# Kernel tuning notes

Measured on AMD Instinct MI355X. Metric: run time of the kernel, lower is better.

The kernel has to match this reference:

```python
import jax, jax.numpy as jnp
import numpy as np

N = 120_000      # points
D = 64           # voxel grid resolution per axis
HID = 96         # hidden_dim
IN = 96          # input_dim
C = HID + IN     # 192, conv input channels
EPS = 1e-5       # BatchNorm eps


def _build_geometry(rng):
    """Precompute the hash-map lookups torchsparse builds on the fly."""
    pts = rng.uniform(0, D - 1e-3, size=(N, 3)).astype(np.float32)
    vox = np.floor(pts).astype(np.int64)                      # voxel coord per point
    flat = (vox[:, 0] * D + vox[:, 1]) * D + vox[:, 2]
    uniq, seg = np.unique(flat, return_inverse=True)          # occupied voxels
    M = uniq.shape[0]
    lut = -np.ones(D * D * D, dtype=np.int64)
    lut[uniq] = np.arange(M)
    ux, uy, uz = uniq // (D * D), (uniq // D) % D, uniq % D
    # 27 kernel offsets for the 3x3x3 sparse conv
    offs = np.array([(dx, dy, dz) for dx in (-1, 0, 1)
                     for dy in (-1, 0, 1) for dz in (-1, 0, 1)], dtype=np.int64)
    nx = ux[:, None] + offs[None, :, 0]
    ny = uy[:, None] + offs[None, :, 1]
    nz = uz[:, None] + offs[None, :, 2]
    ok = (nx >= 0) & (nx < D) & (ny >= 0) & (ny < D) & (nz >= 0) & (nz < D)
    nflat = (np.clip(nx, 0, D - 1) * D + np.clip(ny, 0, D - 1)) * D + np.clip(nz, 0, D - 1)
    nbr = np.where(ok, lut[nflat], -1)
    nbr = np.where(nbr < 0, M, nbr).astype(np.int32)          # row M = zero pad
    # 8 trilinear corners for devoxelization
    frac = pts - vox
    coffs = np.array([(a, b, c) for a in (0, 1) for b in (0, 1) for c in (0, 1)], dtype=np.int64)
    cx = vox[:, 0:1] + coffs[None, :, 0]
    cy = vox[:, 1:2] + coffs[None, :, 1]
    cz = vox[:, 2:3] + coffs[None, :, 2]
    okc = (cx < D) & (cy < D) & (cz < D)
    cflat = (np.clip(cx, 0, D - 1) * D + np.clip(cy, 0, D - 1)) * D + np.clip(cz, 0, D - 1)
    cidx = np.where(okc, lut[cflat], -1)
    w = np.ones((N, 8), dtype=np.float32)
    for k in range(8):
        for d in range(3):
            w[:, k] *= frac[:, d] if coffs[k, d] == 1 else (1.0 - frac[:, d])
    w = np.where(cidx >= 0, w, 0.0).astype(np.float32)        # missing voxel -> weight 0
    cidx = np.where(cidx < 0, M, cidx).astype(np.int32)
    return seg.astype(np.int32), nbr, cidx, w


def setup_inputs() -> dict:
    rng = np.random.default_rng(0)
    seg, nbr, cidx, cw = _build_geometry(rng)
    key = jax.random.key(0)
    ks = jax.random.split(key, 4)
    return {
        "hidden_F": jax.random.normal(ks[0], (N, HID), jnp.float32),
        "query_F": jax.random.normal(ks[1], (N, IN), jnp.float32),
        "W_conv": jax.random.normal(ks[2], (27, C, HID), jnp.float32) * (1.0 / np.sqrt(27.0 * C)),
        "gamma": jnp.ones((HID,), jnp.float32),
        "beta": jnp.zeros((HID,), jnp.float32),
        "W_lin": jax.random.normal(ks[3], (C, IN), jnp.float32) * (1.0 / np.sqrt(C)),
        "b_lin": jnp.zeros((IN,), jnp.float32),
        "corner_w": jnp.asarray(cw),
        "seg_ids": jnp.asarray(seg),
        "nbr_idx": jnp.asarray(nbr),
        "corner_idx": jnp.asarray(cidx),
    }


def reference(hidden_F, query_F, W_conv, gamma, beta, W_lin, b_lin, corner_w,
              seg_ids, nbr_idx, corner_idx):
    M = nbr_idx.shape[0]
    hx = jnp.concatenate([hidden_F, query_F], axis=1)                  # [N, C]
    # initial_voxelize: scatter-mean point features into occupied voxels
    vsum = jax.ops.segment_sum(hx, seg_ids, num_segments=M)            # [M, C]
    cnt = jax.ops.segment_sum(jnp.ones((hx.shape[0], 1), hx.dtype),
                              seg_ids, num_segments=M)
    vfeat = vsum / jnp.maximum(cnt, 1.0)
    # sparse 3x3x3 conv: gather 27 hashed neighbors (row M is zero pad)
    vpad = jnp.concatenate([vfeat, jnp.zeros((1, C), vfeat.dtype)], axis=0)
    acc = jnp.zeros((M, HID), vfeat.dtype)
    for k in range(27):  # fixed small kernel loop
        acc = acc + vpad[nbr_idx[:, k]] @ W_conv[k]
    # BatchNorm (batch stats over occupied voxels) + ReLU
    mu = jnp.mean(acc, axis=0)
    var = jnp.mean((acc - mu) ** 2, axis=0)
    y = jax.nn.relu(gamma * (acc - mu) * jax.lax.rsqrt(var + EPS) + beta)
    # voxel_to_point(nearest=False): trilinear 8-corner gather
    ypad = jnp.concatenate([y, jnp.zeros((1, HID), y.dtype)], axis=0)
    out = jnp.zeros((hx.shape[0], HID), y.dtype)
    for k in range(8):  # fixed corner loop
        out = out + corner_w[:, k:k + 1] * ypad[corner_idx[:, k]]
    # residual point transform: out.F + Linear(hx.F)
    return out + hx @ W_lin + b_lin
```

## Files before the change

### kernel.cpp

```cpp
#include <hip/hip_runtime.h>
#include <hip/hip_bf16.h>
#include <cstdint>

typedef __bf16 bf16;
typedef __bf16 bf16x8 __attribute__((ext_vector_type(8)));
typedef __bf16 bf16x4 __attribute__((ext_vector_type(4)));
typedef float f32x4 __attribute__((ext_vector_type(4)));
typedef int i32x4 __attribute__((ext_vector_type(4)));

#define HIDC 96
#define CINC 192
#define EPSC 1e-5f

#define STG_B 20480
#define STG_ELEM 10240

#define GLD_LDS16(g, l)                                                        \
  __builtin_amdgcn_global_load_lds(                                            \
      (const __attribute__((address_space(1))) void*)(g),                      \
      (__attribute__((address_space(3))) void*)(l), 16, 0, 0)

__global__ void k_repack(const float* __restrict__ Wc, const float* __restrict__ Wl,
                         bf16* __restrict__ dst, int total) {
  int t = blockIdx.x * 256 + threadIdx.x;
  if (t >= total) return;
  int off = t / 18432;
  int rem = t - off * 18432;
  int cix = rem >> 9;
  int lane = (rem >> 3) & 63;
  int j = rem & 7;
  int k = (cix / 6) * 32 + ((lane >> 4) << 3) + j;
  int col = (cix % 6) * 16 + (lane & 15);
  const float* src = (off < 27) ? (Wc + ((size_t)off * CINC + k) * HIDC + col)
                                : (Wl + (size_t)k * HIDC + col);
  int half = (cix >= 18) ? 1 : 0;
  size_t de = (size_t)(off * 2 + half) * STG_ELEM + (size_t)(rem - half * 9216);
  dst[de] = (bf16)(*src);
}

__global__ void k_count(const int* __restrict__ seg, int* __restrict__ cnt, int Npts) {
  int t = blockIdx.x * 256 + threadIdx.x;
  if (t < Npts) atomicAdd(cnt + seg[t], 1);
}

__global__ void k_bsum(const int* __restrict__ cnt, int* __restrict__ bsum, int M) {
  __shared__ int sm[256];
  int i = blockIdx.x * 256 + threadIdx.x;
  sm[threadIdx.x] = (i < M) ? cnt[i] : 0;
  __syncthreads();
  for (int st = 128; st > 0; st >>= 1) {
    if (threadIdx.x < st) sm[threadIdx.x] += sm[threadIdx.x + st];
    __syncthreads();
  }
  if (threadIdx.x == 0) bsum[blockIdx.x] = sm[0];
}

__global__ void k_bscan(int* __restrict__ bsum, int nb) {
  __shared__ int sm[1024];
  int i = threadIdx.x;
  int v = (i < nb) ? bsum[i] : 0;
  sm[i] = v;
  __syncthreads();
  for (int st = 1; st < 1024; st <<= 1) {
    int t = (i >= st) ? sm[i - st] : 0;
    __syncthreads();
    sm[i] += t;
    __syncthreads();
  }
  if (i < nb) bsum[i] = sm[i] - v;
}

__global__ void k_ptr(const int* __restrict__ cnt, const int* __restrict__ bsum,
                      int* __restrict__ ptr, int* __restrict__ cursor, int M) {
  __shared__ int sm[256];
  int i = blockIdx.x * 256 + threadIdx.x;
  int v = (i < M) ? cnt[i] : 0;
  sm[threadIdx.x] = v;
  __syncthreads();
  for (int st = 1; st < 256; st <<= 1) {
    int t = (threadIdx.x >= st) ? sm[threadIdx.x - st] : 0;
    __syncthreads();
    sm[threadIdx.x] += t;
    __syncthreads();
  }
  if (i < M) {
    int e = bsum[blockIdx.x] + sm[threadIdx.x] - v;
    ptr[i] = e;
    cursor[i] = e;
  }
}

__global__ void k_scatter(const int* __restrict__ seg, int* __restrict__ cursor,
                          int* __restrict__ plist, int Npts) {
  int t = blockIdx.x * 256 + threadIdx.x;
  if (t < Npts) {
    int pos = atomicAdd(cursor + seg[t], 1);
    plist[pos] = t;
  }
}

__global__ void k_gmean(const float* __restrict__ hid, const float* __restrict__ qry,
                        const int* __restrict__ ptr, const int* __restrict__ cnt,
                        const int* __restrict__ plist, bf16* __restrict__ vpad, int M) {
  int t = blockIdx.x * 256 + threadIdx.x;
  if (t >= (M + 1) * 48) return;
  int v = t / 48;
  int q = t - v * 48;
  f32x4 a = {0.f, 0.f, 0.f, 0.f};
  if (v < M) {
    int st = ptr[v], n = cnt[v];
    const float* base = (q < 24) ? (hid + q * 4) : (qry + (q - 24) * 4);
    for (int j = 0; j < n; j++) {
      int p = plist[st + j];
      a += *(const f32x4*)(base + (size_t)p * HIDC);
    }
    a *= (1.0f / (float)(n > 0 ? n : 1));
  }
  bf16x4 o;
#pragma unroll
  for (int j = 0; j < 4; j++) o[j] = (bf16)a[j];
  *(bf16x4*)(vpad + (size_t)v * CINC + q * 4) = o;
}

__launch_bounds__(256, 4)
__global__ void k_conv(const bf16* __restrict__ vpad, const int* __restrict__ nbr,
                       const bf16* __restrict__ wpack, float* __restrict__ accbuf,
                       float* __restrict__ bnsum, int M, int nblk, int nper) {
  const int bx = (int)(blockIdx.x & 7) * nper + (int)(blockIdx.x >> 3);
  if (bx >= nblk) return;
  __shared__ __align__(16) char smem[40960];
  const int tid = threadIdx.x;
  const int wave = tid >> 6;
  const int lane = tid & 63;
  const int m = lane & 15;
  const int quad = lane >> 4;
  const int rb = bx * 128 + wave * 32;

  f32x4 acc[2][6];
#pragma unroll
  for (int rt = 0; rt < 2; rt++)
#pragma unroll
    for (int ct = 0; ct < 6; ct++) {
      f32x4 z = {0.f, 0.f, 0.f, 0.f};
      acc[rt][ct] = z;
    }

  const char* wb = (const char*)wpack;

  {
    char* dstb = smem;
#pragma unroll
    for (int i = 0; i < 5; i++) {
      const int base = wave * 1024 + i * 4096;
      GLD_LDS16(wb + base + lane * 16, dstb + base);
    }
  }
  int gidx[2], gidx2[2];
#pragma unroll
  for (int rt = 0; rt < 2; rt++) {
    int r = rb + rt * 16 + m;
    gidx[rt] = (r < M) ? nbr[(size_t)r * 27] : M;
  }
  bf16x8 afn[2][3];
#pragma unroll
  for (int kc2 = 0; kc2 < 3; kc2++)
#pragma unroll
    for (int rt = 0; rt < 2; rt++)
      afn[rt][kc2] = *(const bf16x8*)(vpad + (size_t)gidx[rt] * CINC + kc2 * 32 + quad * 8);
  __builtin_amdgcn_s_barrier();

  for (int s = 0; s < 54; s++) {
    const int buf = s & 1;
    const int half = s & 1;
    const int off = s >> 1;
    if (half == 0) {
      const int offn = off + 1;
#pragma unroll
      for (int rt = 0; rt < 2; rt++) {
        int r = rb + rt * 16 + m;
        gidx2[rt] = (r < M && offn < 27) ? nbr[(size_t)r * 27 + offn] : M;
      }
    }
    if (s < 53) {
      const char* src = wb + (size_t)(s + 1) * STG_B;
      char* dstb = smem + (buf ^ 1) * STG_B;
#pragma unroll
      for (int i = 0; i < 5; i++) {
        const int base = wave * 1024 + i * 4096;
        GLD_LDS16(src + base + lane * 16, dstb + base);
      }
    }
    __builtin_amdgcn_sched_barrier(0);

    bf16x8 afc[2][3];
#pragma unroll
    for (int kc2 = 0; kc2 < 3; kc2++)
#pragma unroll
      for (int rt = 0; rt < 2; rt++) afc[rt][kc2] = afn[rt][kc2];

    const char* bbr = smem + buf * STG_B;
#pragma unroll
    for (int kc2 = 0; kc2 < 3; kc2++) {
#pragma unroll
      for (int ct = 0; ct < 6; ct++) {
        bf16x8 bfm = *(const bf16x8*)(bbr + (size_t)(kc2 * 6 + ct) * 1024 + (size_t)lane * 16);
#pragma unroll
        for (int rt = 0; rt < 2; rt++)
          acc[rt][ct] = __builtin_amdgcn_mfma_f32_16x16x32_bf16(afc[rt][kc2], bfm, acc[rt][ct], 0, 0, 0);
      }
      if (s < 53) {
        if (half == 0) {
#pragma unroll
          for (int rt = 0; rt < 2; rt++)
            afn[rt][kc2] = *(const bf16x8*)(vpad + (size_t)gidx[rt] * CINC +
                                            (kc2 + 3) * 32 + quad * 8);
        } else {
#pragma unroll
          for (int rt = 0; rt < 2; rt++)
            afn[rt][kc2] = *(const bf16x8*)(vpad + (size_t)gidx2[rt] * CINC +
                                            kc2 * 32 + quad * 8);
        }
      }
    }
    if (half == 1) {
      gidx[0] = gidx2[0];
      gidx[1] = gidx2[1];
    }
    asm volatile("s_waitcnt vmcnt(6)" ::: "memory");
    __builtin_amdgcn_s_barrier();
  }

  float ps[6], pq[6];
#pragma unroll
  for (int ct = 0; ct < 6; ct++) { ps[ct] = 0.f; pq[ct] = 0.f; }
#pragma unroll
  for (int rt = 0; rt < 2; rt++)
#pragma unroll
    for (int rr = 0; rr < 4; rr++) {
      const int r2 = rb + rt * 16 + quad * 4 + rr;
      if (r2 < M) {
#pragma unroll
        for (int ct = 0; ct < 6; ct++) {
          float v = acc[rt][ct][rr];
          ps[ct] += v;
          pq[ct] += v * v;
        }
      }
    }
#pragma unroll
  for (int ct = 0; ct < 6; ct++) {
    float s1 = ps[ct], s2 = pq[ct];
    s1 += __shfl_xor(s1, 16);
    s2 += __shfl_xor(s2, 16);
    s1 += __shfl_xor(s1, 32);
    s2 += __shfl_xor(s2, 32);
    if (quad == 0) {
      atomicAdd(bnsum + ct * 16 + m, s1);
      atomicAdd(bnsum + 96 + ct * 16 + m, s2);
    }
  }
  float(*trw)[98] = (float(*)[98])(smem + wave * (16 * 98 * 4));
  const int erow = lane >> 3;
  const int ecb = (lane & 7) * 4;
#pragma unroll
  for (int rt = 0; rt < 2; rt++) {
#pragma unroll
    for (int ct = 0; ct < 6; ct++)
#pragma unroll
      for (int rr = 0; rr < 4; rr++)
        trw[quad * 4 + rr][ct * 16 + m] = acc[rt][ct][rr];
#pragma unroll
    for (int rh = 0; rh < 2; rh++) {
      const int row = rh * 8 + erow;
      const int r2 = rb + rt * 16 + row;
      if (r2 < M) {
#pragma unroll
        for (int it = 0; it < 3; it++) {
          f32x4 v = *(const f32x4*)&trw[row][it * 32 + ecb];
          *(f32x4*)(accbuf + (size_t)r2 * HIDC + it * 32 + ecb) = v;
        }
      }
    }
  }
}

__global__ void k_bnapply(const float* __restrict__ accbuf, const float* __restrict__ bnsum,
                          const float* __restrict__ gamma, const float* __restrict__ beta,
                          bf16* __restrict__ ypad, int M) {
  __shared__ float ssc[96], ssh[96];
  if (threadIdx.x < 96) {
    int c = threadIdx.x;
    float inv = 1.0f / (float)M;
    float mu = bnsum[c] * inv;
    float var = fmaxf(bnsum[96 + c] * inv - mu * mu, 0.f);
    float sc = gamma[c] * rsqrtf(var + EPSC);
    ssc[c] = sc;
    ssh[c] = beta[c] - mu * sc;
  }
  __syncthreads();
  int t = blockIdx.x * 256 + threadIdx.x;
  if (t >= (M + 1) * 24) return;
  int v = t / 24;
  int g = t - v * 24;
  f32x4 y = {0.f, 0.f, 0.f, 0.f};
  if (v < M) {
    f32x4 a = *(const f32x4*)(accbuf + (size_t)v * HIDC + g * 4);
#pragma unroll
    for (int j = 0; j < 4; j++) y[j] = fmaxf(a[j] * ssc[g * 4 + j] + ssh[g * 4 + j], 0.f);
  }
  bf16x4 o;
#pragma unroll
  for (int j = 0; j < 4; j++) o[j] = (bf16)y[j];
  *(bf16x4*)(ypad + (size_t)v * HIDC + g * 4) = o;
}

__launch_bounds__(256, 4)
__global__ void k_linear(const float* __restrict__ hid, const float* __restrict__ qry,
                         const bf16* __restrict__ wlpack, const float* __restrict__ blin,
                         bf16* __restrict__ lin, int Npts) {
  const int tid = threadIdx.x;
  const int wave = tid >> 6;
  const int lane = tid & 63;
  const int m = lane & 15;
  const int quad = lane >> 4;
  const int rb = blockIdx.x * 128 + wave * 32;

  f32x4 acc[2][6];
#pragma unroll
  for (int rt = 0; rt < 2; rt++)
#pragma unroll
    for (int ct = 0; ct < 6; ct++) {
      f32x4 z = {0.f, 0.f, 0.f, 0.f};
      acc[rt][ct] = z;
    }

  int prow[2];
#pragma unroll
  for (int rt = 0; rt < 2; rt++) {
    int r = rb + rt * 16 + m;
    prow[rt] = (r < Npts) ? r : (Npts - 1);
  }
  const char* wp = (const char*)wlpack;
#pragma unroll
  for (int kc = 0; kc < 6; kc++) {
    const float* srcA = (kc < 3) ? (hid + kc * 32) : (qry + (kc - 3) * 32);
    bf16x8 af[2];
#pragma unroll
    for (int rt = 0; rt < 2; rt++) {
      const float* pA = srcA + (size_t)prow[rt] * HIDC + quad * 8;
      f32x4 lo = *(const f32x4*)pA;
      f32x4 hi = *(const f32x4*)(pA + 4);
#pragma unroll
      for (int j = 0; j < 4; j++) {
        af[rt][j] = (bf16)lo[j];
        af[rt][4 + j] = (bf16)hi[j];
      }
    }
    const int half = (kc >= 3) ? 1 : 0;
    const int kcl = kc - half * 3;
#pragma unroll
    for (int ct = 0; ct < 6; ct++) {
      bf16x8 bfm = *(const bf16x8*)(wp + (size_t)half * STG_B +
                                    (size_t)((kcl * 6 + ct) * 64 + lane) * 16);
#pragma unroll
      for (int rt = 0; rt < 2; rt++)
        acc[rt][ct] = __builtin_amdgcn_mfma_f32_16x16x32_bf16(af[rt], bfm, acc[rt][ct], 0, 0, 0);
    }
  }
  float bl[6];
#pragma unroll
  for (int ct = 0; ct < 6; ct++) bl[ct] = blin[ct * 16 + m];
#pragma unroll
  for (int rt = 0; rt < 2; rt++)
#pragma unroll
    for (int rr = 0; rr < 4; rr++) {
      const int r2 = rb + rt * 16 + quad * 4 + rr;
      if (r2 < Npts) {
        bf16* dst = lin + (size_t)r2 * HIDC + m;
#pragma unroll
        for (int ct = 0; ct < 6; ct++)
          dst[ct * 16] = (bf16)(acc[rt][ct][rr] + bl[ct]);
      }
    }
}

__global__ void k_out(const bf16* __restrict__ lin, const bf16* __restrict__ ypad,
                      const float* __restrict__ cw, const int* __restrict__ cidx,
                      float* __restrict__ out, int Npts) {
  int t = blockIdx.x * 256 + threadIdx.x;
  if (t >= Npts * 12) return;
  int p = t / 12;
  int g = t - p * 12;
  float a[8];
  bf16x8 lv = *(const bf16x8*)(lin + (size_t)p * HIDC + g * 8);
#pragma unroll
  for (int j = 0; j < 8; j++) a[j] = (float)lv[j];
  f32x4 w0 = *(const f32x4*)(cw + (size_t)p * 8);
  f32x4 w1 = *(const f32x4*)(cw + (size_t)p * 8 + 4);
  const i32x4* cp = (const i32x4*)(cidx + (size_t)p * 8);
  i32x4 c0 = cp[0], c1 = cp[1];
#pragma unroll
  for (int k = 0; k < 8; k++) {
    int idx = (k < 4) ? c0[k] : c1[k - 4];
    float wk = (k < 4) ? w0[k] : w1[k - 4];
    bf16x8 yv = *(const bf16x8*)(ypad + (size_t)idx * HIDC + g * 8);
#pragma unroll
    for (int j = 0; j < 8; j++) a[j] += wk * (float)yv[j];
  }
  float* op = out + (size_t)p * HIDC + g * 8;
  f32x4 s0, s1;
#pragma unroll
  for (int j = 0; j < 4; j++) { s0[j] = a[j]; s1[j] = a[4 + j]; }
  *(f32x4*)op = s0;
  *(f32x4*)(op + 4) = s1;
}

extern "C" void kernel_launch(void* const* d_in, const int* in_sizes, int n_in,
                              void* d_out, int out_size, void* d_ws, size_t ws_size,
                              hipStream_t stream) {
  const float* hid = (const float*)d_in[0];
  const float* qry = (const float*)d_in[1];
  const float* Wc = (const float*)d_in[2];
  const float* gamma = (const float*)d_in[3];
  const float* beta = (const float*)d_in[4];
  const float* Wl = (const float*)d_in[5];
  const float* blin = (const float*)d_in[6];
  const float* cw = (const float*)d_in[7];
  const int* seg = (const int*)d_in[8];
  const int* nbr = (const int*)d_in[9];
  const int* cidx = (const int*)d_in[10];
  float* out = (float*)d_out;
  const int Npts = in_sizes[0] / HIDC;
  const int M = in_sizes[9] / 27;

  char* ws = (char*)d_ws;
  size_t cur = 0;
  auto alloc = [&](size_t b) { size_t o = cur; cur = (cur + b + 255) & ~(size_t)255; return o; };
  size_t o_cnt = alloc((size_t)M * 4);
  size_t o_bn = alloc(192 * 4);
  size_t zend = cur;
  size_t o_ptr = alloc((size_t)M * 4);
  size_t o_cur = alloc((size_t)M * 4);
  size_t o_pl = alloc((size_t)Npts * 4);
  size_t o_bs = alloc(1024 * 4);
  size_t RA = (size_t)M * HIDC * 4;
  size_t needA = (size_t)Npts * HIDC * 2;
  if (needA > RA) RA = needA;
  size_t o_A = alloc(RA);
  size_t o_B = alloc((size_t)(M + 1) * CINC * 2);
  size_t o_wpack = alloc((size_t)56 * STG_B);
  (void)ws_size; (void)n_in; (void)out_size;

  int* cnt = (int*)(ws + o_cnt);
  float* bnsum = (float*)(ws + o_bn);
  int* ptr = (int*)(ws + o_ptr);
  int* cursor = (int*)(ws + o_cur);
  int* plist = (int*)(ws + o_pl);
  int* bsum = (int*)(ws + o_bs);
  float* accbuf = (float*)(ws + o_A);
  bf16* lin = (bf16*)(ws + o_A);
  bf16* vpad = (bf16*)(ws + o_B);
  bf16* ypad = (bf16*)(ws + o_B);
  bf16* wpack = (bf16*)(ws + o_wpack);
  bf16* wlpack = (bf16*)(ws + o_wpack + (size_t)54 * STG_B);

  hipMemsetAsync(ws, 0, zend, stream);

  int totalRepack = 28 * 18432;
  k_repack<<<(totalRepack + 255) / 256, 256, 0, stream>>>(Wc, Wl, wpack, totalRepack);

  int nb = (M + 255) / 256;
  k_count<<<(Npts + 255) / 256, 256, 0, stream>>>(seg, cnt, Npts);
  k_bsum<<<nb, 256, 0, stream>>>(cnt, bsum, M);
  k_bscan<<<1, 1024, 0, stream>>>(bsum, nb);
  k_ptr<<<nb, 256, 0, stream>>>(cnt, bsum, ptr, cursor, M);
  k_scatter<<<(Npts + 255) / 256, 256, 0, stream>>>(seg, cursor, plist, Npts);
  k_gmean<<<(((M + 1) * 48) + 255) / 256, 256, 0, stream>>>(hid, qry, ptr, cnt, plist, vpad, M);

  int nblk = (M + 127) / 128;
  int nper = (nblk + 7) / 8;
  k_conv<<<nper * 8, 256, 0, stream>>>(vpad, nbr, wpack, accbuf, bnsum, M, nblk, nper);
  k_bnapply<<<((M + 1) * 24 + 255) / 256, 256, 0, stream>>>(accbuf, bnsum, gamma, beta, ypad, M);
  k_linear<<<(Npts + 127) / 128, 256, 0, stream>>>(hid, qry, wlpack, blin, lin, Npts);
  k_out<<<(Npts * 12 + 255) / 256, 256, 0, stream>>>(lin, ypad, cw, cidx, out, Npts);
}
```

Before: 420.7 us.

## Stage conv weights through registers, scan with wave shuffles, store accumulators directly

The conv kernel stops using direct global-to-LDS loads for the weight stages. It now prefetches each stage into registers, writes it to a double-buffered LDS array, and syncs with __syncthreads. The accumulator write-out skips the LDS transpose and stores scalars straight to global memory, which gives less coalesced stores but no staging step. The block-sum scan is rewritten with wave shuffles instead of a shared-memory Hillis-Steele loop, and launch bounds drop to 3 waves per SIMD to allow more registers for the prefetch buffer.

```diff
diff --git a/kernel.cpp b/kernel.cpp
--- a/kernel.cpp
+++ b/kernel.cpp
@@ -14,11 +14,6 @@
 
 #define STG_B 20480
 #define STG_ELEM 10240
-
-#define GLD_LDS16(g, l)                                                        \
-  __builtin_amdgcn_global_load_lds(                                            \
-      (const __attribute__((address_space(1))) void*)(g),                      \
-      (__attribute__((address_space(3))) void*)(l), 16, 0, 0)
 
 __global__ void k_repack(const float* __restrict__ Wc, const float* __restrict__ Wl,
                          bf16* __restrict__ dst, int total) {
@@ -56,18 +51,29 @@
 }
 
 __global__ void k_bscan(int* __restrict__ bsum, int nb) {
-  __shared__ int sm[1024];
   int i = threadIdx.x;
   int v = (i < nb) ? bsum[i] : 0;
-  sm[i] = v;
+  int x = v;
+#pragma unroll
+  for (int d = 1; d < 64; d <<= 1) {
+    int t = __shfl_up(x, d);
+    if ((i & 63) >= d) x += t;
+  }
+  __shared__ int wsum[16];
+  if ((i & 63) == 63) wsum[i >> 6] = x;
   __syncthreads();
-  for (int st = 1; st < 1024; st <<= 1) {
-    int t = (i >= st) ? sm[i - st] : 0;
-    __syncthreads();
-    sm[i] += t;
-    __syncthreads();
-  }
-  if (i < nb) bsum[i] = sm[i] - v;
+  if (i < 16) {
+    int w = wsum[i];
+    int y = w;
+#pragma unroll
+    for (int d = 1; d < 16; d <<= 1) {
+      int t = __shfl_up(y, d, 16);
+      if (i >= d) y += t;
+    }
+    wsum[i] = y - w;
+  }
+  __syncthreads();
+  if (i < nb) bsum[i] = (x - v) + wsum[i >> 6];
 }
 
 __global__ void k_ptr(const int* __restrict__ cnt, const int* __restrict__ bsum,
@@ -122,13 +128,13 @@
   *(bf16x4*)(vpad + (size_t)v * CINC + q * 4) = o;
 }
 
-__launch_bounds__(256, 4)
+__launch_bounds__(256, 3)
 __global__ void k_conv(const bf16* __restrict__ vpad, const int* __restrict__ nbr,
                        const bf16* __restrict__ wpack, float* __restrict__ accbuf,
                        float* __restrict__ bnsum, int M, int nblk, int nper) {
   const int bx = (int)(blockIdx.x & 7) * nper + (int)(blockIdx.x >> 3);
   if (bx >= nblk) return;
-  __shared__ __align__(16) char smem[40960];
+  __shared__ bf16 Bb[2][STG_B / 2];
   const int tid = threadIdx.x;
   const int wave = tid >> 6;
   const int lane = tid & 63;
@@ -146,15 +152,11 @@
     }
 
   const char* wb = (const char*)wpack;
-
-  {
-    char* dstb = smem;
-#pragma unroll
-    for (int i = 0; i < 5; i++) {
-      const int base = wave * 1024 + i * 4096;
-      GLD_LDS16(wb + base + lane * 16, dstb + base);
-    }
-  }
+  i32x4 breg[5];
+#pragma unroll
+  for (int i = 0; i < 5; i++)
+    breg[i] = *(const i32x4*)(wb + (size_t)(tid + 256 * i) * 16);
+
   int gidx[2], gidx2[2];
 #pragma unroll
   for (int rt = 0; rt < 2; rt++) {
@@ -167,10 +169,28 @@
 #pragma unroll
     for (int rt = 0; rt < 2; rt++)
       afn[rt][kc2] = *(const bf16x8*)(vpad + (size_t)gidx[rt] * CINC + kc2 * 32 + quad * 8);
-  __builtin_amdgcn_s_barrier();
 
   for (int s = 0; s < 54; s++) {
     const int buf = s & 1;
+    {
+      char* bbw = (char*)&Bb[buf][0];
+#pragma unroll
+      for (int i = 0; i < 5; i++)
+        *(i32x4*)(bbw + (size_t)(tid + 256 * i) * 16) = breg[i];
+    }
+    __syncthreads();
+    if (s < 53) {
+      const char* src = wb + (size_t)(s + 1) * STG_B;
+#pragma unroll
+      for (int i = 0; i < 5; i++)
+        breg[i] = *(const i32x4*)(src + (size_t)(tid + 256 * i) * 16);
+    }
+    bf16x8 afc[2][3];
+#pragma unroll
+    for (int kc2 = 0; kc2 < 3; kc2++)
+#pragma unroll
+      for (int rt = 0; rt < 2; rt++) afc[rt][kc2] = afn[rt][kc2];
+
     const int half = s & 1;
     const int off = s >> 1;
     if (half == 0) {
@@ -180,73 +200,60 @@
         int r = rb + rt * 16 + m;
         gidx2[rt] = (r < M && offn < 27) ? nbr[(size_t)r * 27 + offn] : M;
       }
-    }
-    if (s < 53) {
-      const char* src = wb + (size_t)(s + 1) * STG_B;
-      char* dstb = smem + (buf ^ 1) * STG_B;
-#pragma unroll
-      for (int i = 0; i < 5; i++) {
-        const int base = wave * 1024 + i * 4096;
-        GLD_LDS16(src + base + lane * 16, dstb + base);
-      }
-    }
-    __builtin_amdgcn_sched_barrier(0);
-
-    bf16x8 afc[2][3];
-#pragma unroll
-    for (int kc2 = 0; kc2 < 3; kc2++)
-#pragma unroll
-      for (int rt = 0; rt < 2; rt++) afc[rt][kc2] = afn[rt][kc2];
-
-    const char* bbr = smem + buf * STG_B;
-#pragma unroll
-    for (int kc2 = 0; kc2 < 3; kc2++) {
-#pragma unroll
-      for (int ct = 0; ct < 6; ct++) {
-        bf16x8 bfm = *(const bf16x8*)(bbr + (size_t)(kc2 * 6 + ct) * 1024 + (size_t)lane * 16);
-#pragma unroll
-        for (int rt = 0; rt < 2; rt++)
-          acc[rt][ct] = __builtin_amdgcn_mfma_f32_16x16x32_bf16(afc[rt][kc2], bfm, acc[rt][ct], 0, 0, 0);
-      }
       if (s < 53) {
-        if (half == 0) {
+#pragma unroll
+        for (int kc2 = 0; kc2 < 3; kc2++)
 #pragma unroll
           for (int rt = 0; rt < 2; rt++)
             afn[rt][kc2] = *(const bf16x8*)(vpad + (size_t)gidx[rt] * CINC +
                                             (kc2 + 3) * 32 + quad * 8);
-        } else {
+      }
+    } else {
+      if (s < 53) {
+#pragma unroll
+        for (int kc2 = 0; kc2 < 3; kc2++)
 #pragma unroll
           for (int rt = 0; rt < 2; rt++)
             afn[rt][kc2] = *(const bf16x8*)(vpad + (size_t)gidx2[rt] * CINC +
                                             kc2 * 32 + quad * 8);
-        }
-      }
-    }
-    if (half == 1) {
+      }
       gidx[0] = gidx2[0];
       gidx[1] = gidx2[1];
     }
-    asm volatile("s_waitcnt vmcnt(6)" ::: "memory");
-    __builtin_amdgcn_s_barrier();
+
+    const char* bbr = (const char*)&Bb[buf][0];
+#pragma unroll
+    for (int kc2 = 0; kc2 < 3; kc2++) {
+#pragma unroll
+      for (int ct = 0; ct < 6; ct++) {
+        bf16x8 bfm = *(const bf16x8*)(bbr + (size_t)(kc2 * 6 + ct) * 1024 + (size_t)lane * 16);
+#pragma unroll
+        for (int rt = 0; rt < 2; rt++)
+          acc[rt][ct] = __builtin_amdgcn_mfma_f32_16x16x32_bf16(afc[rt][kc2], bfm, acc[rt][ct], 0, 0, 0);
+      }
+    }
   }
 
   float ps[6], pq[6];
 #pragma unroll
   for (int ct = 0; ct < 6; ct++) { ps[ct] = 0.f; pq[ct] = 0.f; }
 #pragma unroll
-  for (int rt = 0; rt < 2; rt++)
+  for (int rt = 0; rt < 2; rt++) {
 #pragma unroll
     for (int rr = 0; rr < 4; rr++) {
       const int r2 = rb + rt * 16 + quad * 4 + rr;
       if (r2 < M) {
+        float* dst = accbuf + (size_t)r2 * HIDC + m;
 #pragma unroll
         for (int ct = 0; ct < 6; ct++) {
           float v = acc[rt][ct][rr];
+          dst[ct * 16] = v;
           ps[ct] += v;
           pq[ct] += v * v;
         }
       }
     }
+  }
 #pragma unroll
   for (int ct = 0; ct < 6; ct++) {
     float s1 = ps[ct], s2 = pq[ct];
@@ -257,29 +264,6 @@
     if (quad == 0) {
       atomicAdd(bnsum + ct * 16 + m, s1);
       atomicAdd(bnsum + 96 + ct * 16 + m, s2);
-    }
-  }
-  float(*trw)[98] = (float(*)[98])(smem + wave * (16 * 98 * 4));
-  const int erow = lane >> 3;
-  const int ecb = (lane & 7) * 4;
-#pragma unroll
-  for (int rt = 0; rt < 2; rt++) {
-#pragma unroll
-    for (int ct = 0; ct < 6; ct++)
-#pragma unroll
-      for (int rr = 0; rr < 4; rr++)
-        trw[quad * 4 + rr][ct * 16 + m] = acc[rt][ct][rr];
-#pragma unroll
-    for (int rh = 0; rh < 2; rh++) {
-      const int row = rh * 8 + erow;
-      const int r2 = rb + rt * 16 + row;
-      if (r2 < M) {
-#pragma unroll
-        for (int it = 0; it < 3; it++) {
-          f32x4 v = *(const f32x4*)&trw[row][it * 32 + ecb];
-          *(f32x4*)(accbuf + (size_t)r2 * HIDC + it * 32 + ecb) = v;
-        }
-      }
     }
   }
 }
```

Result: no change. 425.6 us (+1.1%).
